# Kernel tuning notes

Measured on AMD Instinct MI355X. Metric: run time of the kernel, lower is better.

Reference implementation:

```python
import jax, jax.numpy as jnp
import numpy as np

B = 65536
NODE, ENUM, ETYPE = 4, 6, 5
XDIM, EDIM, HDIM, ZDIM = 4, 5, 128, 32
ODIM = (2 * NODE + ETYPE) * ENUM  # 78
BETA = 0.005
EPS_SCALE = 0.01


def setup_inputs() -> dict:
    keys = jax.random.split(jax.random.key(0), 64)
    ki = iter(range(64))
    def rn(shape, s=1.0):
        return jax.random.normal(keys[next(ki)], shape, dtype=jnp.float32) * s
    # NAS-Bench-201 DAG edges per graph, batched as disjoint union
    base_src = jnp.array([0, 0, 1, 0, 1, 2], dtype=jnp.int32)
    base_dst = jnp.array([1, 2, 2, 3, 3, 3], dtype=jnp.int32)
    off = (jnp.arange(B, dtype=jnp.int32) * NODE)[:, None]
    edge_index = jnp.stack([(off + base_src).reshape(-1), (off + base_dst).reshape(-1)])
    s = 0.05
    inp = {
        'x': rn((B * NODE, XDIM)),
        'edge_attr': rn((B * ENUM, EDIM)),
        'arch_tensor': jax.random.uniform(keys[next(ki)], (B, ENUM, 2 * NODE + ETYPE), dtype=jnp.float32),
        'eps': rn((B, ZDIM)),
        'edge_index': edge_index,
        # conv0 (xdim=4 -> hdim=128)
        'c0_rw1': rn((XDIM, XDIM), s), 'c0_rb1': jnp.zeros((XDIM,), jnp.float32),
        'c0_rw2': rn((XDIM, HDIM), s), 'c0_rb2': jnp.zeros((HDIM,), jnp.float32),
        'c0_kw': rn((2 * XDIM + EDIM, HDIM), s),
        # conv1, conv2 (128 -> 128)
        'c1_rw1': rn((HDIM, HDIM), s), 'c1_rb1': jnp.zeros((HDIM,), jnp.float32),
        'c1_rw2': rn((HDIM, HDIM), s), 'c1_rb2': jnp.zeros((HDIM,), jnp.float32),
        'c1_kw': rn((2 * HDIM + EDIM, HDIM), s),
        'c2_rw1': rn((HDIM, HDIM), s), 'c2_rb1': jnp.zeros((HDIM,), jnp.float32),
        'c2_rw2': rn((HDIM, HDIM), s), 'c2_rb2': jnp.zeros((HDIM,), jnp.float32),
        'c2_kw': rn((2 * HDIM + EDIM, HDIM), s),
        # VAE heads
        'fc3_w': rn((HDIM, ZDIM), s), 'fc3_b': jnp.zeros((ZDIM,), jnp.float32),
        'fc4_w': rn((HDIM, ZDIM), s), 'fc4_b': jnp.zeros((ZDIM,), jnp.float32),
        'fc5_w': rn((ZDIM, HDIM), s), 'fc5_b': jnp.zeros((HDIM,), jnp.float32),
        # decoder: Resid_MLP(hdim,hdim) -> Resid_MLP(hdim,odim)
        'd1_mw': rn((HDIM, HDIM), s), 'd1_mb': jnp.zeros((HDIM,), jnp.float32),
        'd1_rw': rn((HDIM, HDIM), s), 'd1_rb': jnp.zeros((HDIM,), jnp.float32),
        'd2_mw': rn((HDIM, ODIM), s), 'd2_mb': jnp.zeros((ODIM,), jnp.float32),
        'd2_rw': rn((HDIM, ODIM), s), 'd2_rb': jnp.zeros((ODIM,), jnp.float32),
    }
    return inp


def _ce(logits, labels):
    # mean cross-entropy over batch*edges, like F.cross_entropy(..., reduction='mean')
    ls = jax.nn.log_softmax(logits, axis=-1)
    return -jnp.mean(jnp.take_along_axis(ls, labels[..., None], axis=-1))


def reference(x, edge_attr, arch_tensor, eps, edge_index,
              c0_rw1, c0_rb1, c0_rw2, c0_rb2, c0_kw,
              c1_rw1, c1_rb1, c1_rw2, c1_rb2, c1_kw,
              c2_rw1, c2_rb1, c2_rw2, c2_rb2, c2_kw,
              fc3_w, fc3_b, fc4_w, fc4_b, fc5_w, fc5_b,
              d1_mw, d1_mb, d1_rw, d1_rb, d2_mw, d2_mb, d2_rw, d2_rb):
    src, dst = edge_index[0], edge_index[1]
    n_nodes = x.shape[0]

    def conv(h, rw1, rb1, rw2, rb2, kw):
        resid = (h @ rw1 + rb1) @ rw2 + rb2  # residual_mlp: two Linears, no activation
        # message: leaky_relu(Linear(cat[x_i(target), x_j(source), edge_attr]))
        m = jax.nn.leaky_relu(jnp.concatenate([h[dst], h[src], edge_attr], axis=1) @ kw)
        return resid + jax.ops.segment_sum(m, dst, num_segments=n_nodes)  # aggr='add'

    h = conv(x, c0_rw1, c0_rb1, c0_rw2, c0_rb2, c0_kw)
    h = conv(h, c1_rw1, c1_rb1, c1_rw2, c1_rb2, c1_kw)
    h = conv(h, c2_rw1, c2_rb1, c2_rw2, c2_rb2, c2_kw)

    hg = h.reshape(B, NODE, HDIM).sum(axis=1)  # sum-pool nodes per graph
    mu = hg @ fc3_w + fc3_b
    logvar = hg @ fc4_w + fc4_b

    # reparameterize (training): z = (eps*eps_scale)*std + mu
    z = eps * EPS_SCALE * jnp.exp(0.5 * logvar) + mu

    # decode
    Hg = jnp.tanh(z @ fc5_w + fc5_b)
    h1 = jax.nn.leaky_relu(Hg @ d1_mw + d1_mb) + (Hg @ d1_rw + d1_rb)
    pred = jax.nn.leaky_relu(h1 @ d2_mw + d2_mb) + (h1 @ d2_rw + d2_rb)
    pred = pred.reshape(B, ENUM, 2 * NODE + ETYPE)
    in_pred, out_pred, et_pred = pred[:, :, :NODE], pred[:, :, NODE:2 * NODE], pred[:, :, 2 * NODE:]

    ti = jnp.argmax(arch_tensor[:, :, :NODE], axis=2)
    to = jnp.argmax(arch_tensor[:, :, NODE:2 * NODE], axis=2)
    te = jnp.argmax(arch_tensor[:, :, 2 * NODE:], axis=2)

    res = _ce(et_pred, te) + _ce(in_pred, ti) + _ce(out_pred, to)
    kld = -0.5 * jnp.mean(1.0 + logvar - mu ** 2 - jnp.exp(logvar))
    return res + BETA * kld
```

## Files before the change

### kernel.cpp

```cpp
#include <hip/hip_runtime.h>
#include <hip/hip_bf16.h>

#define BATCH 65536

typedef __bf16 bf16_t;
typedef __bf16 bf16x8 __attribute__((ext_vector_type(8)));
typedef float  f32x4  __attribute__((ext_vector_type(4)));

__device__ __forceinline__ f32x4 mfma16(bf16x8 a, bf16x8 b, f32x4 c) {
    return __builtin_amdgcn_mfma_f32_16x16x32_bf16(a, b, c, 0, 0, 0);
}
__device__ __forceinline__ int swz128(int row, int col) {
    return row * 128 + ((((col >> 3) ^ (row & 7)) << 3) | (col & 7));
}

struct PrepSrcs { const float* p[16]; };

__global__ __launch_bounds__(256) void prep_weights(PrepSrcs ps,
    const float* __restrict__ c0_rb1, const float* __restrict__ c0_rb2,
    const float* __restrict__ c1_rb1, const float* __restrict__ c1_rb2,
    const float* __restrict__ c2_rb1, const float* __restrict__ c2_rb2,
    bf16_t* __restrict__ dst, float* __restrict__ bias)
{
    int f = blockIdx.x;
    if (f >= 368) {
        int c = threadIdx.x;
        if (c < 128) {
            if (f == 368) {
                const float* rw2 = ps.p[11];
                float s = c1_rb2[c];
                for (int m = 0; m < 128; m++) s += c1_rb1[m] * rw2[m * 128 + c];
                bias[c] = s;
            } else if (f == 369) {
                const float* rw2 = ps.p[13];
                float s = c2_rb2[c];
                for (int m = 0; m < 128; m++) s += c2_rb1[m] * rw2[m * 128 + c];
                bias[128 + c] = s;
            } else {
                const float* rw2 = ps.p[15];
                float s = c0_rb2[c];
                for (int m = 0; m < 4; m++) s += c0_rb1[m] * rw2[m * 128 + c];
                bias[256 + c] = s;
            }
        }
        return;
    }
    const int BASE[20] = {0,32,64,96,128,160,192,200,208,216,248,280,300,320,328,336,344,352,360,368};
    const int SRC[19]  = {10,0,0,12,1,1,2,3,4,5,6,7,8,14,9,9,9,0,1};
    const int KTt[19]  = {4,4,4,4,4,4,4,4,1,4,4,4,4,1,1,1,1,1,1};
    const int KLIM[19] = {128,128,128,128,128,128,128,128,32,128,128,128,128,4,4,4,5,5,5};
    const int NLIM[19] = {128,128,128,128,128,128,32,32,128,128,128,78,78,128,128,128,128,128,128};
    const int STR[19]  = {128,128,128,128,128,128,32,32,128,128,128,78,78,128,128,128,128,128,128};
    const int RO[19]   = {0,0,128,0,0,128,0,0,0,0,0,0,0,0,0,4,8,256,256};

    int ei = 0;
    while (ei < 18 && BASE[ei + 1] <= f) ei++;
    int lf = f - BASE[ei];
    int kt = lf % KTt[ei];
    int nt = lf / KTt[ei];
    #pragma unroll
    for (int r2 = 0; r2 < 2; r2++) {
        int idx = threadIdx.x * 2 + r2;
        int l = idx >> 3, j = idx & 7;
        int row = 32 * kt + 8 * (l >> 4) + j;
        int col = 16 * nt + (l & 15);
        float v = 0.f;
        if (ei == 0 || ei == 3) {
            const float* rw1 = ps.p[ei == 0 ? 10 : 12];
            const float* rw2 = ps.p[ei == 0 ? 11 : 13];
            for (int m = 0; m < 128; m++) v += rw1[row * 128 + m] * rw2[m * 128 + col];
        } else if (ei == 13) {
            if (row < 4) {
                const float* rw1 = ps.p[14];
                const float* rw2 = ps.p[15];
                for (int m = 0; m < 4; m++) v += rw1[row * 4 + m] * rw2[m * 128 + col];
            }
        } else {
            if (row < KLIM[ei] && col < NLIM[ei])
                v = ps.p[SRC[ei]][(row + RO[ei]) * STR[ei] + col];
        }
        dst[f * 512 + idx] = (bf16_t)v;
    }
}

__device__ __forceinline__ void edge_update(float o[4], const f32x4& kd, const f32x4& ks,
                                            const float* et)
{
    float mm;
    mm = kd[1] + ks[0] + et[0]; mm = fmaxf(mm, 0.01f * mm); o[1] += mm;
    mm = kd[2] + ks[0] + et[1]; mm = fmaxf(mm, 0.01f * mm); o[2] += mm;
    mm = kd[2] + ks[1] + et[2]; mm = fmaxf(mm, 0.01f * mm); o[2] += mm;
    mm = kd[3] + ks[0] + et[3]; mm = fmaxf(mm, 0.01f * mm); o[3] += mm;
    mm = kd[3] + ks[1] + et[4]; mm = fmaxf(mm, 0.01f * mm); o[3] += mm;
    mm = kd[3] + ks[2] + et[5]; mm = fmaxf(mm, 0.01f * mm); o[3] += mm;
}


template<bool LAST>
__device__ __forceinline__ void conv_pass(
    bf16_t* lA, const bf16x8 aet[3],
    const bf16_t* wf, const bf16_t* wet, const float* b12,
    int w, int q, int lr, int lane)
{
    bf16x8 ah[2][4];
    #pragma unroll
    for (int mt = 0; mt < 2; mt++) {
        int row = 32 * w + 16 * mt + lr;
        #pragma unroll
        for (int kt = 0; kt < 4; kt++)
            ah[mt][kt] = *(const bf16x8*)(lA + row * 128 + (((4 * kt + q) ^ (row & 7)) << 3));
    }
    __syncthreads();

    const bf16_t* wfd = wf + 32 * 512;
    const bf16_t* wfs = wf + 64 * 512;
    #pragma unroll 1
    for (int nt = 0; nt < 8; nt++) {
        int col = 16 * nt + lr;
        const f32x4 zz = {0.f, 0.f, 0.f, 0.f};
        bf16x8 be = *(const bf16x8*)(wet + nt * 512 + lane * 8);
        f32x4 zet0 = mfma16(aet[0], be, zz);
        f32x4 zet1 = mfma16(aet[1], be, zz);
        f32x4 zetB = mfma16(aet[2], be, zz);
        float bv = b12[col];
        f32x4 rr[2], kd[2], ks[2];
        rr[0] = (f32x4){bv, bv, bv, bv}; rr[1] = rr[0];
        kd[0] = zz; kd[1] = zz;
        ks[0] = zz; ks[1] = zz;
        #pragma unroll
        for (int kt = 0; kt < 4; kt++) {
            bf16x8 bw = *(const bf16x8*)(wf  + (nt * 4 + kt) * 512 + lane * 8);
            bf16x8 bd = *(const bf16x8*)(wfd + (nt * 4 + kt) * 512 + lane * 8);
            bf16x8 bs = *(const bf16x8*)(wfs + (nt * 4 + kt) * 512 + lane * 8);
            #pragma unroll
            for (int mt = 0; mt < 2; mt++) {
                rr[mt] = mfma16(ah[mt][kt], bw, rr[mt]);
                kd[mt] = mfma16(ah[mt][kt], bd, kd[mt]);
                ks[mt] = mfma16(ah[mt][kt], bs, ks[mt]);
            }
        }
        #pragma unroll
        for (int mt = 0; mt < 2; mt++) {
            int el = 8 * w + 4 * mt + q;
            f32x4 zA = mt ? zet1 : zet0;
            float et6[6] = {zA[0], zA[1], zA[2], zA[3],
                            mt ? zetB[2] : zetB[0], mt ? zetB[3] : zetB[1]};
            float o[4] = {rr[mt][0], rr[mt][1], rr[mt][2], rr[mt][3]};
            edge_update(o, kd[mt], ks[mt], et6);
            if (!LAST) {
                #pragma unroll
                for (int j = 0; j < 4; j++)
                    lA[swz128(32 * w + 16 * mt + 4 * q + j, col)] = (bf16_t)o[j];
            } else {
                lA[swz128(el, col)] = (bf16_t)(o[0] + o[1] + o[2] + o[3]);
            }
        }
    }
    __syncthreads();
}

__device__ __forceinline__ float ce_group(const float* p, const float* a, int off, int len) {
    float m = p[off];
    #pragma unroll
    for (int i = 1; i < 5; i++) if (i < len) m = fmaxf(m, p[off + i]);
    float am = a[off]; int lbl = 0;
    #pragma unroll
    for (int i = 1; i < 5; i++) if (i < len) { float av = a[off + i]; if (av > am) { am = av; lbl = i; } }
    float s = 0.f;
    #pragma unroll
    for (int i = 0; i < 5; i++) if (i < len) s += __expf(p[off + i] - m);
    return (m + __logf(s)) - p[off + lbl];
}

__global__ __launch_bounds__(256, 3) void fused_kernel(
    const float* __restrict__ x, const float* __restrict__ ea,
    const float* __restrict__ arch, const float* __restrict__ eps,
    const bf16_t* __restrict__ wfr, const float* __restrict__ bias,
    const float* __restrict__ fc3_b, const float* __restrict__ fc4_b,
    const float* __restrict__ fc5_b, const float* __restrict__ d1_mb,
    const float* __restrict__ d1_rb, const float* __restrict__ d2_mb,
    const float* __restrict__ d2_rb,
    float* __restrict__ ce_part, float* __restrict__ kld_part)
{
    __shared__ __align__(16) bf16_t lA[128 * 128];
    __shared__ __align__(16) float  lred[8];

    const int tid = threadIdx.x;
    const int w = tid >> 6, lane = tid & 63, q = lane >> 4, lr = lane & 15;
    const int e0 = blockIdx.x * 32;
    const int r0 = e0 * 4;

    bf16x8 aet[3];
    #pragma unroll
    for (int t = 0; t < 3; t++) {
        bf16x8 a = {0, 0, 0, 0, 0, 0, 0, 0};
        if (q == 0) {
            int el_w, u;
            if (t < 2) { el_w = 4 * t + (lr >> 2); u = lr & 3; }
            else       { el_w = 4 * ((lr >> 1) & 1) + (lr >> 2); u = 4 + (lr & 1); }
            const float* pe = ea + (size_t)((e0 + 8 * w + el_w) * 6 + u) * 5;
            #pragma unroll
            for (int i = 0; i < 5; i++) a[i] = (bf16_t)pe[i];
        }
        aet[t] = a;
    }

    {
        bf16x8 ax[2];
        #pragma unroll
        for (int mt = 0; mt < 2; mt++) {
            float4 xv = {0.f, 0.f, 0.f, 0.f};
            if (q == 0) xv = *(const float4*)(x + (size_t)(r0 + 32 * w + 16 * mt + lr) * 4);
            bf16x8 a = {0, 0, 0, 0, 0, 0, 0, 0};
            a[0] = (bf16_t)xv.x; a[1] = (bf16_t)xv.y; a[2] = (bf16_t)xv.z; a[3] = (bf16_t)xv.w;
            ax[mt] = a;
        }
        const bf16_t* w0f = wfr + 320 * 512;
        const bf16_t* wdf = wfr + 328 * 512;
        const bf16_t* wsf = wfr + 336 * 512;
        const bf16_t* wef = wfr + 344 * 512;
        const float* b0 = bias + 256;
        #pragma unroll 1
        for (int nt = 0; nt < 8; nt++) {
            int col = 16 * nt + lr;
            const f32x4 zz = {0.f, 0.f, 0.f, 0.f};
            bf16x8 be = *(const bf16x8*)(wef + nt * 512 + lane * 8);
            f32x4 zet0 = mfma16(aet[0], be, zz);
            f32x4 zet1 = mfma16(aet[1], be, zz);
            f32x4 zetB = mfma16(aet[2], be, zz);
            float bb = b0[col];
            f32x4 rr[2], kd[2], ks[2];
            rr[0] = (f32x4){bb, bb, bb, bb}; rr[1] = rr[0];
            kd[0] = zz; kd[1] = zz;
            ks[0] = zz; ks[1] = zz;
            bf16x8 bw0 = *(const bf16x8*)(w0f + nt * 512 + lane * 8);
            bf16x8 bwa = *(const bf16x8*)(wdf + nt * 512 + lane * 8);
            bf16x8 bwb = *(const bf16x8*)(wsf + nt * 512 + lane * 8);
            #pragma unroll
            for (int mt = 0; mt < 2; mt++) {
                rr[mt] = mfma16(ax[mt], bw0, rr[mt]);
                kd[mt] = mfma16(ax[mt], bwa, kd[mt]);
                ks[mt] = mfma16(ax[mt], bwb, ks[mt]);
            }
            #pragma unroll
            for (int mt = 0; mt < 2; mt++) {
                f32x4 zA = mt ? zet1 : zet0;
                float et6[6] = {zA[0], zA[1], zA[2], zA[3],
                                mt ? zetB[2] : zetB[0], mt ? zetB[3] : zetB[1]};
                float o[4] = {rr[mt][0], rr[mt][1], rr[mt][2], rr[mt][3]};
                edge_update(o, kd[mt], ks[mt], et6);
                #pragma unroll
                for (int j = 0; j < 4; j++)
                    lA[swz128(32 * w + 16 * mt + 4 * q + j, col)] = (bf16_t)o[j];
            }
        }
    }
    __syncthreads();

    conv_pass<false>(lA, aet, wfr,            wfr + 352 * 512, bias,       w, q, lr, lane);
    conv_pass<true >(lA, aet, wfr + 96 * 512, wfr + 360 * 512, bias + 128, w, q, lr, lane);

    const int mtd = w >> 1, tp = w & 1;
    const int grow = 16 * mtd + lr;

    bf16x8 ag[4];
    #pragma unroll
    for (int kt = 0; kt < 4; kt++)
        ag[kt] = *(const bf16x8*)(lA + grow * 128 + (((4 * kt + q) ^ (grow & 7)) << 3));
    float bmu = fc3_b[16 * tp + lr], blv = fc4_b[16 * tp + lr];
    f32x4 amu = (f32x4){bmu, bmu, bmu, bmu}, alv = (f32x4){blv, blv, blv, blv};
    const bf16_t* f3 = wfr + (192 + tp * 4) * 512;
    const bf16_t* f4 = wfr + (200 + tp * 4) * 512;
    #pragma unroll
    for (int kt = 0; kt < 4; kt++) {
        amu = mfma16(ag[kt], *(const bf16x8*)(f3 + kt * 512 + lane * 8), amu);
        alv = mfma16(ag[kt], *(const bf16x8*)(f4 + kt * 512 + lane * 8), alv);
    }
    float kldp = 0.f;
    bf16_t* lz = lA + 4096;
    #pragma unroll
    for (int j = 0; j < 4; j++) {
        int el = 16 * mtd + 4 * q + j;
        float mu = amu[j], lv = alv[j];
        kldp += 1.f + lv - mu * mu - __expf(lv);
        int c = 16 * tp + lr;
        float zz2 = eps[(size_t)(e0 + el) * 32 + c] * 0.01f * __expf(0.5f * lv) + mu;
        lz[el * 32 + ((((c >> 3) ^ (el & 3)) << 3) | (c & 7))] = (bf16_t)zz2;
    }
    __syncthreads();

    bf16_t* lHg = lA + 6144;
    bf16x8 az = *(const bf16x8*)(lz + grow * 32 + ((q ^ (grow & 3)) << 3));
    const bf16_t* f5 = wfr + 208 * 512;
    #pragma unroll 1
    for (int i = 0; i < 4; i++) {
        int nt = 4 * tp + i;
        float b = fc5_b[16 * nt + lr];
        f32x4 a = (f32x4){b, b, b, b};
        a = mfma16(az, *(const bf16x8*)(f5 + nt * 512 + lane * 8), a);
        #pragma unroll
        for (int j = 0; j < 4; j++) {
            float ex2 = __expf(2.f * a[j]);
            float th = 1.f - 2.f / (ex2 + 1.f);
            lHg[swz128(16 * mtd + 4 * q + j, 16 * nt + lr)] = (bf16_t)th;
        }
    }
    __syncthreads();

    bf16x8 aHg[4];
    #pragma unroll
    for (int kt = 0; kt < 4; kt++)
        aHg[kt] = *(const bf16x8*)(lHg + grow * 128 + (((4 * kt + q) ^ (grow & 7)) << 3));
    const bf16_t* wd1m = wfr + 216 * 512;
    const bf16_t* wd1r = wfr + 248 * 512;
    #pragma unroll 1
    for (int i = 0; i < 4; i++) {
        int nt = 4 * tp + i;
        int col = 16 * nt + lr;
        float bm = d1_mb[col], br = d1_rb[col];
        f32x4 am = (f32x4){bm, bm, bm, bm}, ar = (f32x4){br, br, br, br};
        #pragma unroll
        for (int kt = 0; kt < 4; kt++) {
            am = mfma16(aHg[kt], *(const bf16x8*)(wd1m + (nt * 4 + kt) * 512 + lane * 8), am);
            ar = mfma16(aHg[kt], *(const bf16x8*)(wd1r + (nt * 4 + kt) * 512 + lane * 8), ar);
        }
        #pragma unroll
        for (int j = 0; j < 4; j++) {
            float v = fmaxf(am[j], 0.01f * am[j]) + ar[j];
            lA[swz128(16 * mtd + 4 * q + j, col)] = (bf16_t)v;
        }
    }
    __syncthreads();

    bf16x8 a1[4];
    #pragma unroll
    for (int kt = 0; kt < 4; kt++)
        a1[kt] = *(const bf16x8*)(lA + grow * 128 + (((4 * kt + q) ^ (grow & 7)) << 3));
    float* lpred = (float*)(lA + 10240);
    const bf16_t* wd2m = wfr + 280 * 512;
    const bf16_t* wd2r = wfr + 300 * 512;
    const int ntbeg = tp ? 3 : 0, ntend = tp ? 5 : 3;
    #pragma unroll 1
    for (int nt = ntbeg; nt < ntend; nt++) {
        int col = 16 * nt + lr;
        float bm = (col < 78) ? d2_mb[col] : 0.f;
        float br = (col < 78) ? d2_rb[col] : 0.f;
        f32x4 pm = (f32x4){bm, bm, bm, bm}, pr = (f32x4){br, br, br, br};
        #pragma unroll
        for (int kt = 0; kt < 4; kt++) {
            pm = mfma16(a1[kt], *(const bf16x8*)(wd2m + (nt * 4 + kt) * 512 + lane * 8), pm);
            pr = mfma16(a1[kt], *(const bf16x8*)(wd2r + (nt * 4 + kt) * 512 + lane * 8), pr);
        }
        #pragma unroll
        for (int j = 0; j < 4; j++) {
            float v = fmaxf(pm[j], 0.01f * pm[j]) + pr[j];
            lpred[(16 * mtd + 4 * q + j) * 80 + col] = v;
        }
    }
    __syncthreads();

    float ces = 0.f;
    if (tid < 192) {
        int el = tid / 6, u = tid - el * 6;
        const float* pa = arch + ((size_t)(e0 + el) * 6 + u) * 13;
        const float* pp = lpred + el * 80 + u * 13;
        ces  = ce_group(pp, pa, 0, 4);
        ces += ce_group(pp, pa, 4, 4);
        ces += ce_group(pp, pa, 8, 5);
    }
    #pragma unroll
    for (int m2 = 1; m2 < 64; m2 <<= 1) {
        ces  += __shfl_xor(ces, m2, 64);
        kldp += __shfl_xor(kldp, m2, 64);
    }
    if (lane == 0) { lred[w] = ces; lred[4 + w] = kldp; }
    __syncthreads();
    if (tid == 0) {
        ce_part[blockIdx.x]  = lred[0] + lred[1] + lred[2] + lred[3];
        kld_part[blockIdx.x] = lred[4] + lred[5] + lred[6] + lred[7];
    }
}

__global__ __launch_bounds__(256) void final_reduce(
    const float* __restrict__ ce_part, const float* __restrict__ kld_part,
    float* __restrict__ out)
{
    __shared__ float r[256];
    int tid = threadIdx.x;
    float c = 0.f, k = 0.f;
    for (int i = tid; i < 2048; i += 256) { c += ce_part[i]; k += kld_part[i]; }
    r[tid] = c; __syncthreads();
    for (int s = 128; s > 0; s >>= 1) { if (tid < s) r[tid] += r[tid + s]; __syncthreads(); }
    float ctot = r[0];
    __syncthreads();
    r[tid] = k; __syncthreads();
    for (int s = 128; s > 0; s >>= 1) { if (tid < s) r[tid] += r[tid + s]; __syncthreads(); }
    if (tid == 0) {
        float ktot = r[0];
        out[0] = ctot / (65536.f * 6.f) - 0.5f * 0.005f * (ktot / (65536.f * 32.f));
    }
}

extern "C" void kernel_launch(void* const* d_in, const int* in_sizes, int n_in,
                              void* d_out, int out_size, void* d_ws, size_t ws_size,
                              hipStream_t stream)
{
    const float* x      = (const float*)d_in[0];
    const float* ea     = (const float*)d_in[1];
    const float* arch   = (const float*)d_in[2];
    const float* eps    = (const float*)d_in[3];
    const float* c0_rw1 = (const float*)d_in[5];
    const float* c0_rb1 = (const float*)d_in[6];
    const float* c0_rw2 = (const float*)d_in[7];
    const float* c0_rb2 = (const float*)d_in[8];
    const float* c0_kw  = (const float*)d_in[9];
    const float* c1_rw1 = (const float*)d_in[10];
    const float* c1_rb1 = (const float*)d_in[11];
    const float* c1_rw2 = (const float*)d_in[12];
    const float* c1_rb2 = (const float*)d_in[13];
    const float* c1_kw  = (const float*)d_in[14];
    const float* c2_rw1 = (const float*)d_in[15];
    const float* c2_rb1 = (const float*)d_in[16];
    const float* c2_rw2 = (const float*)d_in[17];
    const float* c2_rb2 = (const float*)d_in[18];
    const float* c2_kw  = (const float*)d_in[19];
    const float* fc3_w  = (const float*)d_in[20];
    const float* fc3_b  = (const float*)d_in[21];
    const float* fc4_w  = (const float*)d_in[22];
    const float* fc4_b  = (const float*)d_in[23];
    const float* fc5_w  = (const float*)d_in[24];
    const float* fc5_b  = (const float*)d_in[25];
    const float* d1_mw  = (const float*)d_in[26];
    const float* d1_mb  = (const float*)d_in[27];
    const float* d1_rw  = (const float*)d_in[28];
    const float* d1_rb  = (const float*)d_in[29];
    const float* d2_mw  = (const float*)d_in[30];
    const float* d2_mb  = (const float*)d_in[31];
    const float* d2_rw  = (const float*)d_in[32];
    const float* d2_rb  = (const float*)d_in[33];

    bf16_t* wfr      = (bf16_t*)d_ws;
    float*  bias     = (float*)((char*)d_ws + 376832);
    float*  ce_part  = (float*)((char*)d_ws + 378368);
    float*  kld_part = (float*)((char*)d_ws + 386560);

    PrepSrcs ps;
    ps.p[0] = c1_kw;  ps.p[1] = c2_kw;  ps.p[2] = fc3_w;  ps.p[3] = fc4_w;
    ps.p[4] = fc5_w;  ps.p[5] = d1_mw;  ps.p[6] = d1_rw;  ps.p[7] = d2_mw;
    ps.p[8] = d2_rw;  ps.p[9] = c0_kw;  ps.p[10] = c1_rw1; ps.p[11] = c1_rw2;
    ps.p[12] = c2_rw1; ps.p[13] = c2_rw2; ps.p[14] = c0_rw1; ps.p[15] = c0_rw2;

    prep_weights<<<371, 256, 0, stream>>>(ps, c0_rb1, c0_rb2, c1_rb1, c1_rb2,
                                          c2_rb1, c2_rb2, wfr, bias);
    fused_kernel<<<BATCH / 32, 256, 0, stream>>>(
        x, ea, arch, eps, wfr, bias,
        fc3_b, fc4_b, fc5_b, d1_mb, d1_rb, d2_mb, d2_rb,
        ce_part, kld_part);
    final_reduce<<<1, 256, 0, stream>>>(ce_part, kld_part, (float*)d_out);
}
```

Baseline: 127.3 us.

## Partition conv passes by output columns with register-resident weights and ping-pong LDS

Each wave now owns two output-column tiles and keeps all their weight fragments in registers, iterating over all eight row tiles read from LDS. Before, each wave owned rows and reloaded every weight tile from global memory. Activations move between two LDS buffers instead of one, and edge-attribute fragments are staged in LDS. This cuts repeated global weight loads and the read-then-barrier step inside each pass. In exchange it roughly doubles LDS use and register pressure, so occupancy drops from 3 to 2 blocks per CU.

```diff
diff --git a/kernel.cpp b/kernel.cpp
--- a/kernel.cpp
+++ b/kernel.cpp
@@ -95,64 +95,68 @@
     mm = kd[3] + ks[2] + et[5]; mm = fmaxf(mm, 0.01f * mm); o[3] += mm;
 }
 
-
 template<bool LAST>
 __device__ __forceinline__ void conv_pass(
-    bf16_t* lA, const bf16x8 aet[3],
+    const bf16_t* bufIn, bf16_t* bufOut, const bf16_t* eaf,
     const bf16_t* wf, const bf16_t* wet, const float* b12,
     int w, int q, int lr, int lane)
 {
-    bf16x8 ah[2][4];
-    #pragma unroll
-    for (int mt = 0; mt < 2; mt++) {
-        int row = 32 * w + 16 * mt + lr;
-        #pragma unroll
-        for (int kt = 0; kt < 4; kt++)
-            ah[mt][kt] = *(const bf16x8*)(lA + row * 128 + (((4 * kt + q) ^ (row & 7)) << 3));
-    }
-    __syncthreads();
-
     const bf16_t* wfd = wf + 32 * 512;
     const bf16_t* wfs = wf + 64 * 512;
+    const int nt0 = 2 * w;
+
+    bf16x8 Bw[2][4], Bd[2][4], Bs[2][4], Be[2];
+    #pragma unroll
+    for (int t = 0; t < 2; t++) {
+        int nt = nt0 + t;
+        #pragma unroll
+        for (int kt = 0; kt < 4; kt++) {
+            Bw[t][kt] = *(const bf16x8*)(wf  + (nt * 4 + kt) * 512 + lane * 8);
+            Bd[t][kt] = *(const bf16x8*)(wfd + (nt * 4 + kt) * 512 + lane * 8);
+            Bs[t][kt] = *(const bf16x8*)(wfs + (nt * 4 + kt) * 512 + lane * 8);
+        }
+        Be[t] = *(const bf16x8*)(wet + nt * 512 + lane * 8);
+    }
+    float bv[2] = {b12[16 * nt0 + lr], b12[16 * nt0 + 16 + lr]};
+    const f32x4 zz = {0.f, 0.f, 0.f, 0.f};
+    f32x4 zB[2] = {zz, zz};
+
     #pragma unroll 1
-    for (int nt = 0; nt < 8; nt++) {
-        int col = 16 * nt + lr;
-        const f32x4 zz = {0.f, 0.f, 0.f, 0.f};
-        bf16x8 be = *(const bf16x8*)(wet + nt * 512 + lane * 8);
-        f32x4 zet0 = mfma16(aet[0], be, zz);
-        f32x4 zet1 = mfma16(aet[1], be, zz);
-        f32x4 zetB = mfma16(aet[2], be, zz);
-        float bv = b12[col];
-        f32x4 rr[2], kd[2], ks[2];
-        rr[0] = (f32x4){bv, bv, bv, bv}; rr[1] = rr[0];
-        kd[0] = zz; kd[1] = zz;
-        ks[0] = zz; ks[1] = zz;
-        #pragma unroll
-        for (int kt = 0; kt < 4; kt++) {
-            bf16x8 bw = *(const bf16x8*)(wf  + (nt * 4 + kt) * 512 + lane * 8);
-            bf16x8 bd = *(const bf16x8*)(wfd + (nt * 4 + kt) * 512 + lane * 8);
-            bf16x8 bs = *(const bf16x8*)(wfs + (nt * 4 + kt) * 512 + lane * 8);
+    for (int mt = 0; mt < 8; mt++) {
+        int arow = 16 * mt + lr;
+        bf16x8 ah[4];
+        #pragma unroll
+        for (int kt = 0; kt < 4; kt++)
+            ah[kt] = *(const bf16x8*)(bufIn + arow * 128 + (((4 * kt + q) ^ (arow & 7)) << 3));
+        bf16x8 aet1 = *(const bf16x8*)(eaf + mt * 512 + lane * 8);
+        if ((mt & 1) == 0) {
+            bf16x8 aetB = *(const bf16x8*)(eaf + (8 + (mt >> 1)) * 512 + lane * 8);
+            zB[0] = mfma16(aetB, Be[0], zz);
+            zB[1] = mfma16(aetB, Be[1], zz);
+        }
+        #pragma unroll
+        for (int t = 0; t < 2; t++) {
+            f32x4 z1 = mfma16(aet1, Be[t], zz);
+            f32x4 rr = (f32x4){bv[t], bv[t], bv[t], bv[t]};
+            f32x4 kd = zz, ks = zz;
             #pragma unroll
-            for (int mt = 0; mt < 2; mt++) {
-                rr[mt] = mfma16(ah[mt][kt], bw, rr[mt]);
-                kd[mt] = mfma16(ah[mt][kt], bd, kd[mt]);
-                ks[mt] = mfma16(ah[mt][kt], bs, ks[mt]);
-            }
-        }
-        #pragma unroll
-        for (int mt = 0; mt < 2; mt++) {
-            int el = 8 * w + 4 * mt + q;
-            f32x4 zA = mt ? zet1 : zet0;
-            float et6[6] = {zA[0], zA[1], zA[2], zA[3],
-                            mt ? zetB[2] : zetB[0], mt ? zetB[3] : zetB[1]};
-            float o[4] = {rr[mt][0], rr[mt][1], rr[mt][2], rr[mt][3]};
-            edge_update(o, kd[mt], ks[mt], et6);
+            for (int kt = 0; kt < 4; kt++) {
+                rr = mfma16(ah[kt], Bw[t][kt], rr);
+                kd = mfma16(ah[kt], Bd[t][kt], kd);
+                ks = mfma16(ah[kt], Bs[t][kt], ks);
+            }
+            int col = 16 * (nt0 + t) + lr;
+            float et6[6] = {z1[0], z1[1], z1[2], z1[3],
+                            (mt & 1) ? zB[t][2] : zB[t][0],
+                            (mt & 1) ? zB[t][3] : zB[t][1]};
+            float o[4] = {rr[0], rr[1], rr[2], rr[3]};
+            edge_update(o, kd, ks, et6);
             if (!LAST) {
                 #pragma unroll
                 for (int j = 0; j < 4; j++)
-                    lA[swz128(32 * w + 16 * mt + 4 * q + j, col)] = (bf16_t)o[j];
+                    bufOut[swz128(16 * mt + 4 * q + j, col)] = (bf16_t)o[j];
             } else {
-                lA[swz128(el, col)] = (bf16_t)(o[0] + o[1] + o[2] + o[3]);
+                bufOut[swz128(4 * mt + q, col)] = (bf16_t)(o[0] + o[1] + o[2] + o[3]);
             }
         }
     }
@@ -172,7 +176,7 @@
     return (m + __logf(s)) - p[off + lbl];
 }
 
-__global__ __launch_bounds__(256, 3) void fused_kernel(
+__global__ __launch_bounds__(256, 2) void fused_kernel(
     const float* __restrict__ x, const float* __restrict__ ea,
     const float* __restrict__ arch, const float* __restrict__ eps,
     const bf16_t* __restrict__ wfr, const float* __restrict__ bias,
@@ -182,86 +186,101 @@
     const float* __restrict__ d2_rb,
     float* __restrict__ ce_part, float* __restrict__ kld_part)
 {
-    __shared__ __align__(16) bf16_t lA[128 * 128];
-    __shared__ __align__(16) float  lred[8];
+    __shared__ __align__(16) bf16_t buf0[128 * 128];
+    __shared__ __align__(16) bf16_t buf1[128 * 128];
+    __shared__ __align__(16) bf16_t eaf[12 * 512];
 
     const int tid = threadIdx.x;
     const int w = tid >> 6, lane = tid & 63, q = lane >> 4, lr = lane & 15;
     const int e0 = blockIdx.x * 32;
     const int r0 = e0 * 4;
 
-    bf16x8 aet[3];
-    #pragma unroll
-    for (int t = 0; t < 3; t++) {
+    {
+        #pragma unroll
+        for (int g = 0; g < 2; g++) {
+            int mt = 4 * g + w;
+            bf16x8 a = {0, 0, 0, 0, 0, 0, 0, 0};
+            if (q == 0) {
+                int el = 4 * mt + (lr >> 2), u = lr & 3;
+                const float* pe = ea + (size_t)((e0 + el) * 6 + u) * 5;
+                #pragma unroll
+                for (int i = 0; i < 5; i++) a[i] = (bf16_t)pe[i];
+            }
+            *(bf16x8*)(eaf + mt * 512 + lane * 8) = a;
+        }
         bf16x8 a = {0, 0, 0, 0, 0, 0, 0, 0};
         if (q == 0) {
-            int el_w, u;
-            if (t < 2) { el_w = 4 * t + (lr >> 2); u = lr & 3; }
-            else       { el_w = 4 * ((lr >> 1) & 1) + (lr >> 2); u = 4 + (lr & 1); }
-            const float* pe = ea + (size_t)((e0 + 8 * w + el_w) * 6 + u) * 5;
+            int v = lr & 3;
+            int el = 4 * (2 * w + (v >> 1)) + (lr >> 2);
+            int u = 4 + (v & 1);
+            const float* pe = ea + (size_t)((e0 + el) * 6 + u) * 5;
             #pragma unroll
             for (int i = 0; i < 5; i++) a[i] = (bf16_t)pe[i];
         }
-        aet[t] = a;
-    }
+        *(bf16x8*)(eaf + (8 + w) * 512 + lane * 8) = a;
+    }
+    __syncthreads();
 
     {
-        bf16x8 ax[2];
-        #pragma unroll
-        for (int mt = 0; mt < 2; mt++) {
-            float4 xv = {0.f, 0.f, 0.f, 0.f};
-            if (q == 0) xv = *(const float4*)(x + (size_t)(r0 + 32 * w + 16 * mt + lr) * 4);
-            bf16x8 a = {0, 0, 0, 0, 0, 0, 0, 0};
-            a[0] = (bf16_t)xv.x; a[1] = (bf16_t)xv.y; a[2] = (bf16_t)xv.z; a[3] = (bf16_t)xv.w;
-            ax[mt] = a;
-        }
         const bf16_t* w0f = wfr + 320 * 512;
         const bf16_t* wdf = wfr + 328 * 512;
         const bf16_t* wsf = wfr + 336 * 512;
         const bf16_t* wef = wfr + 344 * 512;
         const float* b0 = bias + 256;
+        const int nt0 = 2 * w;
+        bf16x8 Bw0[2], Bd0[2], Bs0[2], Be0[2];
+        #pragma unroll
+        for (int t = 0; t < 2; t++) {
+            int nt = nt0 + t;
+            Bw0[t] = *(const bf16x8*)(w0f + nt * 512 + lane * 8);
+            Bd0[t] = *(const bf16x8*)(wdf + nt * 512 + lane * 8);
+            Bs0[t] = *(const bf16x8*)(wsf + nt * 512 + lane * 8);
+            Be0[t] = *(const bf16x8*)(wef + nt * 512 + lane * 8);
+        }
+        float bv[2] = {b0[16 * nt0 + lr], b0[16 * nt0 + 16 + lr]};
+        const f32x4 zz = {0.f, 0.f, 0.f, 0.f};
+        f32x4 zB[2] = {zz, zz};
         #pragma unroll 1
-        for (int nt = 0; nt < 8; nt++) {
-            int col = 16 * nt + lr;
-            const f32x4 zz = {0.f, 0.f, 0.f, 0.f};
-            bf16x8 be = *(const bf16x8*)(wef + nt * 512 + lane * 8);
-            f32x4 zet0 = mfma16(aet[0], be, zz);
-            f32x4 zet1 = mfma16(aet[1], be, zz);
-            f32x4 zetB = mfma16(aet[2], be, zz);
-            float bb = b0[col];
-            f32x4 rr[2], kd[2], ks[2];
-            rr[0] = (f32x4){bb, bb, bb, bb}; rr[1] = rr[0];
-            kd[0] = zz; kd[1] = zz;
-            ks[0] = zz; ks[1] = zz;
-            bf16x8 bw0 = *(const bf16x8*)(w0f + nt * 512 + lane * 8);
-            bf16x8 bwa = *(const bf16x8*)(wdf + nt * 512 + lane * 8);
-            bf16x8 bwb = *(const bf16x8*)(wsf + nt * 512 + lane * 8);
+        for (int mt = 0; mt < 8; mt++) {
+            bf16x8 ax = {0, 0, 0, 0, 0, 0, 0, 0};
+            if (q == 0) {
+                float4 xv = *(const float4*)(x + (size_t)(r0 + 16 * mt + lr) * 4);
+                ax[0] = (bf16_t)xv.x; ax[1] = (bf16_t)xv.y;
+                ax[2] = (bf16_t)xv.z; ax[3] = (bf16_t)xv.w;
+            }
+            bf16x8 aet1 = *(const bf16x8*)(eaf + mt * 512 + lane * 8);
+            if ((mt & 1) == 0) {
+                bf16x8 aetB = *(const bf16x8*)(eaf + (8 + (mt >> 1)) * 512 + lane * 8);
+                zB[0] = mfma16(aetB, Be0[0], zz);
+                zB[1] = mfma16(aetB, Be0[1], zz);
+            }
             #pragma unroll
-            for (int mt = 0; mt < 2; mt++) {
-                rr[mt] = mfma16(ax[mt], bw0, rr[mt]);
-                kd[mt] = mfma16(ax[mt], bwa, kd[mt]);
-                ks[mt] = mfma16(ax[mt], bwb, ks[mt]);
-            }
-            #pragma unroll
-            for (int mt = 0; mt < 2; mt++) {
-                f32x4 zA = mt ? zet1 : zet0;
-                float et6[6] = {zA[0], zA[1], zA[2], zA[3],
-                                mt ? zetB[2] : zetB[0], mt ? zetB[3] : zetB[1]};
-                float o[4] = {rr[mt][0], rr[mt][1], rr[mt][2], rr[mt][3]};
-                edge_update(o, kd[mt], ks[mt], et6);
+            for (int t = 0; t < 2; t++) {
+                f32x4 z1 = mfma16(aet1, Be0[t], zz);
+                f32x4 rr = (f32x4){bv[t], bv[t], bv[t], bv[t]};
+                f32x4 kd = mfma16(ax, Bd0[t], zz);
+                f32x4 ks = mfma16(ax, Bs0[t], zz);
+                rr = mfma16(ax, Bw0[t], rr);
+                int col = 16 * (nt0 + t) + lr;
+                float et6[6] = {z1[0], z1[1], z1[2], z1[3],
+                                (mt & 1) ? zB[t][2] : zB[t][0],
+                                (mt & 1) ? zB[t][3] : zB[t][1]};
+                float o[4] = {rr[0], rr[1], rr[2], rr[3]};
+                edge_update(o, kd, ks, et6);
                 #pragma unroll
                 for (int j = 0; j < 4; j++)
-                    lA[swz128(32 * w + 16 * mt + 4 * q + j, col)] = (bf16_t)o[j];
-            }
-        }
-    }
-    __syncthreads();
-
-    conv_pass<false>(lA, aet, wfr,            wfr + 352 * 512, bias,       w, q, lr, lane);
-    conv_pass<true >(lA, aet, wfr + 96 * 512, wfr + 360 * 512, bias + 128, w, q, lr, lane);
+                    buf0[swz128(16 * mt + 4 * q + j, col)] = (bf16_t)o[j];
+            }
+        }
+    }
+    __syncthreads();
+
+    conv_pass<false>(buf0, buf1, eaf, wfr,            wfr + 352 * 512, bias,       w, q, lr, lane);
+    conv_pass<true >(buf1, buf0, eaf, wfr + 96 * 512, wfr + 360 * 512, bias + 128, w, q, lr, lane);
 
     const int mtd = w >> 1, tp = w & 1;
     const int grow = 16 * mtd + lr;
+    bf16_t* lA = buf0;
 
     bf16x8 ag[4];
     #pragma unroll
@@ -373,6 +392,7 @@
         ces  += __shfl_xor(ces, m2, 64);
         kldp += __shfl_xor(kldp, m2, 64);
     }
+    float* lred = (float*)eaf;
     if (lane == 0) { lred[w] = ces; lred[4 + w] = kldp; }
     __syncthreads();
     if (tid == 0) {
```

New measurement: 136.5 us. 7.2% more time.
